# Performance work log

Hardware: AMD Instinct MI355X
Metric: run time of the kernel (lower is better)

The kernel has to match this reference:

```python
import jax, jax.numpy as jnp
import numpy as np

HIDDEN = 4096
N_HEADS = 32
N_KV_HEADS = 8
HEAD_DIM = HIDDEN // N_HEADS  # 128
ROPE_THETA = 10000.0
NEG_INF = -1e9


def rotate_half(x):
    x1, x2 = jnp.split(x, 2, axis=-1)
    return jnp.concatenate([-x2, x1], axis=-1)


def rope_cos_sin(seq_len, dim, dtype):
    inv_freq = 1.0 / (ROPE_THETA ** (jnp.arange(0, dim, 2, dtype=jnp.float32) / dim))
    t = jnp.arange(seq_len, dtype=jnp.float32)
    freqs = jnp.outer(t, inv_freq)              # (S, dim/2)
    emb = jnp.concatenate([freqs, freqs], -1)   # (S, dim)
    return jnp.cos(emb).astype(dtype), jnp.sin(emb).astype(dtype)


def setup_inputs() -> dict:
    key = jax.random.key(0)
    ks = jax.random.split(key, 5)
    B, S = 2, 2048
    hidden_states = jax.random.normal(ks[0], (B, S, HIDDEN), jnp.float32)
    # additive causal mask (B, 1, S, S)
    causal = jnp.triu(jnp.full((S, S), NEG_INF, jnp.float32), k=1)
    attention_mask = jnp.broadcast_to(causal[None, None], (B, 1, S, S))
    scale = 0.02
    wq = jax.random.normal(ks[1], (HIDDEN, HIDDEN), jnp.float32) * scale
    wk = jax.random.normal(ks[2], (N_KV_HEADS * HEAD_DIM, HIDDEN), jnp.float32) * scale
    wv = jax.random.normal(ks[3], (N_KV_HEADS * HEAD_DIM, HIDDEN), jnp.float32) * scale
    wo = jax.random.normal(ks[4], (HIDDEN, HIDDEN), jnp.float32) * scale
    return {"hidden_states": hidden_states, "attention_mask": attention_mask,
            "wq": wq, "wk": wk, "wv": wv, "wo": wo}


def reference(hidden_states, attention_mask, wq, wk, wv, wo):
    B, S, _ = hidden_states.shape
    H, Hk, D = N_HEADS, N_KV_HEADS, HEAD_DIM
    G = H // Hk  # kv groups

    q = (hidden_states @ wq.T).reshape(B, S, H, D).transpose(0, 2, 1, 3)   # (B,H,S,D)
    k = (hidden_states @ wk.T).reshape(B, S, Hk, D).transpose(0, 2, 1, 3)  # (B,Hk,S,D)
    v = (hidden_states @ wv.T).reshape(B, S, Hk, D).transpose(0, 2, 1, 3)

    cos, sin = rope_cos_sin(S, D, hidden_states.dtype)  # (S,D)
    cos = cos[None, None]  # (1,1,S,D)
    sin = sin[None, None]
    q = q * cos + rotate_half(q) * sin
    k = k * cos + rotate_half(k) * sin

    # GQA without materializing repeated K/V: view q as (B,Hk,G,S,D)
    qg = q.reshape(B, Hk, G, S, D)
    scores = jnp.einsum('bkgqd,bkld->bkgql', qg, k) / jnp.sqrt(jnp.asarray(D, q.dtype))
    scores = scores + attention_mask[:, :, None]  # (B,1,1,S,S) broadcast
    attn = jax.nn.softmax(scores.astype(jnp.float32), axis=-1).astype(q.dtype)
    out = jnp.einsum('bkgql,bkld->bkgqd', attn, v)  # (B,Hk,G,S,D)
    out = out.reshape(B, H, S, D).transpose(0, 2, 1, 3).reshape(B, S, H * D)
    return out @ wo.T
```

## Files before the change

kernel.cpp:

```cpp
#include <hip/hip_runtime.h>
#include <hip/hip_bf16.h>
#include <stdint.h>


#define HIDDEN 4096
#define NH 32
#define NKV 8
#define HD 128
#define SLEN 2048
#define BATCH 2
#define QKVLD 6144

typedef __attribute__((ext_vector_type(8))) short bf16x8;
typedef __attribute__((ext_vector_type(4))) float f32x4;

__device__ __forceinline__ unsigned short f2bf(float f) {
  __hip_bfloat16 h = __float2bfloat16(f);
  return *reinterpret_cast<unsigned short*>(&h);
}
__device__ __forceinline__ float bf2f(unsigned short h) {
  union { uint32_t u; float f; } v; v.u = ((uint32_t)h) << 16;
  return v.f;
}
__device__ __forceinline__ void gload_lds16(const void* g, void* l) {
  __builtin_amdgcn_global_load_lds(
      (const __attribute__((address_space(1))) unsigned int*)g,
      (__attribute__((address_space(3))) unsigned int*)l, 16, 0, 0);
}

__global__ __launch_bounds__(256) void cvt_f32_bf16(const float* __restrict__ in,
                                                    unsigned short* __restrict__ out) {
  size_t i = ((size_t)blockIdx.x * 256 + threadIdx.x) * 8;
  f32x4 a = *(const f32x4*)&in[i];
  f32x4 b = *(const f32x4*)&in[i + 4];
  bf16x8 o;
#pragma unroll
  for (int j = 0; j < 4; ++j) { o[j] = (short)f2bf(a[j]); o[4 + j] = (short)f2bf(b[j]); }
  *(bf16x8*)&out[i] = o;
}

__device__ __forceinline__ void store_out(unsigned short* C, size_t i, float v) { C[i] = f2bf(v); }
__device__ __forceinline__ void store_out(float* C, size_t i, float v) { C[i] = v; }

template <typename OutT>
__global__ __launch_bounds__(256, 2)
void gemm_bt(const unsigned short* __restrict__ A, const unsigned short* __restrict__ B,
             OutT* __restrict__ C, int M, int N, int K) {
  __shared__ __align__(16) unsigned short Asm[128 * 32];
  __shared__ __align__(16) unsigned short Bsm[128 * 32];
  const int tid = threadIdx.x;
  const int lane = tid & 63, wid = tid >> 6;
  const int lr = lane & 15, lg = lane >> 4;
  const int wr = wid >> 1, wc = wid & 1;

  const int nbn = N >> 7;
  const int nwg = gridDim.x;
  int wg = (int)blockIdx.x;
  wg = (wg & 7) * (nwg >> 3) + (wg >> 3);
  const int bm = wg / nbn, bn = wg % nbn;

  const unsigned short* Ab = A + (size_t)bm * 128 * K;
  const unsigned short* Bb = B + (size_t)bn * 128 * K;

  f32x4 acc[4][4] = {};

  const int c0 = tid, c1 = tid + 256;
  const int ar0 = c0 >> 2, ak0 = (c0 & 3) * 8;
  const int ar1 = c1 >> 2, ak1 = (c1 & 3) * 8;

  for (int kt = 0; kt < K; kt += 32) {
    __syncthreads();
    gload_lds16(Ab + (size_t)ar0 * K + kt + ak0, &Asm[c0 * 8]);
    gload_lds16(Ab + (size_t)ar1 * K + kt + ak1, &Asm[c1 * 8]);
    gload_lds16(Bb + (size_t)ar0 * K + kt + ak0, &Bsm[c0 * 8]);
    gload_lds16(Bb + (size_t)ar1 * K + kt + ak1, &Bsm[c1 * 8]);
    __syncthreads();

    bf16x8 af[4], bfr[4];
#pragma unroll
    for (int mi = 0; mi < 4; ++mi)
      af[mi] = *(const bf16x8*)&Asm[(wr * 64 + mi * 16 + lr) * 32 + lg * 8];
#pragma unroll
    for (int ni = 0; ni < 4; ++ni)
      bfr[ni] = *(const bf16x8*)&Bsm[(wc * 64 + ni * 16 + lr) * 32 + lg * 8];
#pragma unroll
    for (int mi = 0; mi < 4; ++mi)
#pragma unroll
      for (int ni = 0; ni < 4; ++ni)
        acc[mi][ni] = __builtin_amdgcn_mfma_f32_16x16x32_bf16(af[mi], bfr[ni], acc[mi][ni], 0, 0, 0);
  }

#pragma unroll
  for (int mi = 0; mi < 4; ++mi)
#pragma unroll
    for (int ni = 0; ni < 4; ++ni)
#pragma unroll
      for (int r = 0; r < 4; ++r) {
        size_t row = (size_t)bm * 128 + wr * 64 + mi * 16 + lg * 4 + r;
        size_t col = (size_t)bn * 128 + wc * 64 + ni * 16 + lr;
        store_out(C, row * N + col, acc[mi][ni][r]);
      }
}

__global__ __launch_bounds__(256) void rope_tables(float* __restrict__ ct, float* __restrict__ st) {
  int idx = blockIdx.x * 256 + threadIdx.x;
  int s = idx >> 6, j = idx & 63;
  float inv = exp2f(-(float)j * (13.287712379549449f / 64.f));
  float f = (float)s * inv;
  ct[idx] = cosf(f);
  st[idx] = sinf(f);
}

__global__ __launch_bounds__(256) void rope_apply(unsigned short* __restrict__ X, int ld,
                                                  const float* __restrict__ ct,
                                                  const float* __restrict__ st, int heads) {
  int idx = blockIdx.x * 256 + threadIdx.x;
  int jc = (idx & 7) * 8;
  int t2 = idx >> 3;
  int hh = t2 % heads;
  int row = t2 / heads;
  int s = row & (SLEN - 1);
  unsigned short* p = X + (size_t)row * ld + hh * HD;
  bf16x8 lo = *(bf16x8*)&p[jc];
  bf16x8 hi = *(bf16x8*)&p[64 + jc];
  bf16x8 nlo, nhi;
#pragma unroll
  for (int j = 0; j < 8; ++j) {
    float c = ct[s * 64 + jc + j];
    float sn = st[s * 64 + jc + j];
    float xl = bf2f((unsigned short)(lo[j]));
    float xh = bf2f((unsigned short)(hi[j]));
    nlo[j] = (short)f2bf(xl * c - xh * sn);
    nhi[j] = (short)f2bf(xh * c + xl * sn);
  }
  *(bf16x8*)&p[jc] = nlo;
  *(bf16x8*)&p[64 + jc] = nhi;
}

__global__ __launch_bounds__(256) void transpose_v(const unsigned short* __restrict__ Vsrc, int ld,
                                                   unsigned short* __restrict__ VT) {
  __shared__ unsigned short tile[64][66];
  const int t = threadIdx.x;
  const int bs = blockIdx.x;
  const int bd = blockIdx.y;
  const int b = bs >> 5;
  const int s0 = (bs & 31) * 64;
  const int d0 = bd * 64;
#pragma unroll
  for (int it = 0; it < 2; ++it) {
    int si = (t >> 3) + it * 32;
    int dj = (t & 7) * 8;
    bf16x8 v = *(const bf16x8*)&Vsrc[(size_t)(b * SLEN + s0 + si) * ld + d0 + dj];
#pragma unroll
    for (int j = 0; j < 8; ++j) tile[si][dj + j] = (unsigned short)(v[j]);
  }
  __syncthreads();
#pragma unroll
  for (int it = 0; it < 2; ++it) {
    int di = (t >> 3) + it * 32;
    int sj = (t & 7) * 8;
    bf16x8 o;
#pragma unroll
    for (int j = 0; j < 8; ++j) o[j] = (short)tile[sj + j][di];
    int c = d0 + di;
    int kvh = c >> 7, d = c & 127;
    *(bf16x8*)&VT[(((size_t)b * NKV + kvh) * HD + d) * SLEN + s0 + sj] = o;
  }
}

__global__ __launch_bounds__(256, 2)
void attn_fwd(const unsigned short* __restrict__ QKV, const unsigned short* __restrict__ VTm,
              unsigned short* __restrict__ Om) {
  const int blk = blockIdx.x;
  const int xcd = blk & 7, jj = blk >> 3;
  const int g = xcd + ((jj >> 5) << 3);
  const int pair = jj & 31;
  const int kvh = g & 7, b = g >> 3;
  const int tid = threadIdx.x;
  const int lane = tid & 63, w = tid >> 6;
  const int lr = lane & 15, lg = lane >> 4;
  const int h = kvh * 4 + w;

  __shared__ __align__(16) unsigned short Ksm[64 * 136];
  __shared__ __align__(16) unsigned short Vsm[128 * 72];
  __shared__ __align__(16) unsigned short Psm[4][32 * 72];
  __shared__ float Alds[4][32];

  const float SL2E = 0.1275378504229740f;

  const unsigned short* Kb0 = QKV + (size_t)(b * SLEN) * QKVLD + 4096 + kvh * HD;
  const unsigned short* VTb = VTm + ((size_t)(b * NKV + kvh) * HD) * SLEN;

#pragma unroll 1
  for (int halfq = 0; halfq < 2; ++halfq) {
    const int qt = halfq ? (63 - pair) : pair;
    const int q0 = qt * 32;
    const int ntiles = (qt >> 1) + 1;

    bf16x8 qf[2][4];
    const unsigned short* Qb = QKV + (size_t)(b * SLEN + q0) * QKVLD + h * HD;
#pragma unroll
    for (int ni = 0; ni < 2; ++ni)
#pragma unroll
      for (int kd = 0; kd < 4; ++kd)
        qf[ni][kd] = *(const bf16x8*)&Qb[(size_t)(ni * 16 + lr) * QKVLD + kd * 32 + lg * 8];

    f32x4 acc_o[2][8] = {};
    float m_run[2] = {-1e30f, -1e30f};
    float l_run[2] = {0.f, 0.f};

    bf16x8 kreg[4], vreg[4];
#pragma unroll
    for (int i = 0; i < 4; ++i) {
      int c = tid + i * 256;
      kreg[i] = *(const bf16x8*)&Kb0[(size_t)(c >> 4) * QKVLD + (c & 15) * 8];
      vreg[i] = *(const bf16x8*)&VTb[(size_t)(c >> 3) * SLEN + (c & 7) * 8];
    }

#pragma unroll 1
    for (int t = 0; t < ntiles; ++t) {
      const int kv0 = t * 64;
      __syncthreads();
#pragma unroll
      for (int i = 0; i < 4; ++i) {
        int c = tid + i * 256;
        *(bf16x8*)&Ksm[(c >> 4) * 136 + (c & 15) * 8] = kreg[i];
        *(bf16x8*)&Vsm[(c >> 3) * 72 + (c & 7) * 8] = vreg[i];
      }
      __syncthreads();

      if (t + 1 < ntiles) {
#pragma unroll
        for (int i = 0; i < 4; ++i) {
          int c = tid + i * 256;
          kreg[i] = *(const bf16x8*)&Kb0[(size_t)(kv0 + 64 + (c >> 4)) * QKVLD + (c & 15) * 8];
          vreg[i] = *(const bf16x8*)&VTb[(size_t)(c >> 3) * SLEN + kv0 + 64 + (c & 7) * 8];
        }
      }

      f32x4 accs[4][2] = {};
#pragma unroll
      for (int kd = 0; kd < 4; ++kd) {
        bf16x8 kf[4];
#pragma unroll
        for (int mi = 0; mi < 4; ++mi)
          kf[mi] = *(const bf16x8*)&Ksm[(mi * 16 + lr) * 136 + kd * 32 + lg * 8];
        __builtin_amdgcn_s_setprio(1);
#pragma unroll
        for (int mi = 0; mi < 4; ++mi)
#pragma unroll
          for (int ni = 0; ni < 2; ++ni)
            accs[mi][ni] =
                __builtin_amdgcn_mfma_f32_16x16x32_bf16(kf[mi], qf[ni][kd], accs[mi][ni], 0, 0, 0);
        __builtin_amdgcn_s_setprio(0);
      }

      const bool domask = (t == ntiles - 1);
      float alpha[2];
#pragma unroll
      for (int ni = 0; ni < 2; ++ni) {
        float cmax = -1e30f;
#pragma unroll
        for (int mi = 0; mi < 4; ++mi)
#pragma unroll
          for (int r = 0; r < 4; ++r) {
            float s = accs[mi][ni][r] * SL2E;
            if (domask) {
              int key = kv0 + mi * 16 + lg * 4 + r;
              int qq = q0 + ni * 16 + lr;
              if (key > qq) s = -1e30f;
            }
            accs[mi][ni][r] = s;
            cmax = fmaxf(cmax, s);
          }
        cmax = fmaxf(cmax, __shfl_xor(cmax, 16));
        cmax = fmaxf(cmax, __shfl_xor(cmax, 32));
        float mnew = fmaxf(m_run[ni], cmax);
        alpha[ni] = exp2f(m_run[ni] - mnew);
        float psum = 0.f;
#pragma unroll
        for (int mi = 0; mi < 4; ++mi)
#pragma unroll
          for (int r = 0; r < 4; ++r) {
            float p = exp2f(accs[mi][ni][r] - mnew);
            accs[mi][ni][r] = p;
            psum += p;
          }
        psum += __shfl_xor(psum, 16);
        psum += __shfl_xor(psum, 32);
        l_run[ni] = l_run[ni] * alpha[ni] + psum;
        m_run[ni] = mnew;
      }

      if (__any(alpha[0] < 1.f) || __any(alpha[1] < 1.f)) {
        if (lg == 0) { Alds[w][lr] = alpha[0]; Alds[w][16 + lr] = alpha[1]; }
        f32x4 al0 = *(const f32x4*)&Alds[w][lg * 4];
        f32x4 al1 = *(const f32x4*)&Alds[w][16 + lg * 4];
#pragma unroll
        for (int nd = 0; nd < 8; ++nd)
#pragma unroll
          for (int r = 0; r < 4; ++r) {
            acc_o[0][nd][r] *= al0[r];
            acc_o[1][nd][r] *= al1[r];
          }
      }

#pragma unroll
      for (int ni = 0; ni < 2; ++ni)
#pragma unroll
        for (int mi = 0; mi < 4; ++mi)
#pragma unroll
          for (int rp = 0; rp < 4; rp += 2) {
            uint32_t pk = (uint32_t)f2bf(accs[mi][ni][rp]) |
                          ((uint32_t)f2bf(accs[mi][ni][rp + 1]) << 16);
            *(uint32_t*)&Psm[w][(ni * 16 + lr) * 72 + mi * 16 + lg * 4 + rp] = pk;
          }

#pragma unroll
      for (int ks = 0; ks < 2; ++ks) {
        bf16x8 pa[2];
#pragma unroll
        for (int pm = 0; pm < 2; ++pm)
          pa[pm] = *(const bf16x8*)&Psm[w][(pm * 16 + lr) * 72 + ks * 32 + lg * 8];
        __builtin_amdgcn_s_setprio(1);
#pragma unroll
        for (int nd = 0; nd < 8; ++nd) {
          bf16x8 vb = *(const bf16x8*)&Vsm[(nd * 16 + lr) * 72 + ks * 32 + lg * 8];
#pragma unroll
          for (int pm = 0; pm < 2; ++pm)
            acc_o[pm][nd] =
                __builtin_amdgcn_mfma_f32_16x16x32_bf16(pa[pm], vb, acc_o[pm][nd], 0, 0, 0);
        }
        __builtin_amdgcn_s_setprio(0);
      }
    }

    if (lg == 0) {
      Alds[w][lr] = 1.f / l_run[0];
      Alds[w][16 + lr] = 1.f / l_run[1];
    }
    f32x4 li0 = *(const f32x4*)&Alds[w][lg * 4];
    f32x4 li1 = *(const f32x4*)&Alds[w][16 + lg * 4];
    unsigned short* Ob = Om + ((size_t)(b * SLEN + q0) * NH + h) * HD;
#pragma unroll
    for (int pm = 0; pm < 2; ++pm)
#pragma unroll
      for (int nd = 0; nd < 8; ++nd)
#pragma unroll
        for (int r = 0; r < 4; ++r) {
          int qq = pm * 16 + lg * 4 + r;
          float v = acc_o[pm][nd][r] * (pm ? li1[r] : li0[r]);
          Ob[(size_t)qq * (NH * HD) + nd * 16 + lr] = f2bf(v);
        }
  }
}

extern "C" void kernel_launch(void* const* d_in, const int* in_sizes, int n_in,
                              void* d_out, int out_size, void* d_ws, size_t ws_size,
                              hipStream_t stream) {
  const float* hidden = (const float*)d_in[0];
  const float* wq = (const float*)d_in[2];
  const float* wk = (const float*)d_in[3];
  const float* wv = (const float*)d_in[4];
  const float* wo = (const float*)d_in[5];

  char* ws = (char*)d_ws;
  const size_t MB = 1ull << 20;
  unsigned short* Xbf  = (unsigned short*)(ws);
  unsigned short* Wqkv = (unsigned short*)(ws + 32 * MB);
  unsigned short* QKV  = (unsigned short*)(ws + 80 * MB);
  unsigned short* Ob   = (unsigned short*)(ws + 128 * MB);
  unsigned short* VTb  = (unsigned short*)(ws + 160 * MB);
  float* ct = (float*)(ws + 168 * MB);
  float* st = (float*)(ws + 168 * MB + 524288);

  cvt_f32_bf16<<<8192, 256, 0, stream>>>(hidden, Xbf);
  cvt_f32_bf16<<<8192, 256, 0, stream>>>(wq, Wqkv);
  cvt_f32_bf16<<<2048, 256, 0, stream>>>(wk, Wqkv + (size_t)4096 * 4096);
  cvt_f32_bf16<<<2048, 256, 0, stream>>>(wv, Wqkv + (size_t)5120 * 4096);

  gemm_bt<unsigned short><<<1536, 256, 0, stream>>>(Xbf, Wqkv, QKV, 4096, 6144, 4096);

  rope_tables<<<512, 256, 0, stream>>>(ct, st);
  rope_apply<<<4096, 256, 0, stream>>>(QKV, QKVLD, ct, st, NH);
  rope_apply<<<1024, 256, 0, stream>>>(QKV + 4096, QKVLD, ct, st, NKV);

  transpose_v<<<dim3(64, 16), 256, 0, stream>>>(QKV + 5120, QKVLD, VTb);

  attn_fwd<<<512, 256, 0, stream>>>(QKV, VTb, Ob);

  cvt_f32_bf16<<<8192, 256, 0, stream>>>(wo, Wqkv);
  gemm_bt<float><<<1024, 256, 0, stream>>>(Ob, Wqkv, (float*)d_out, 4096, 4096, 4096);
}
```

Measured before the change: 650.6 us.

## Use 256x256 GEMM tiles with four-stage LDS prefetch pipeline

Replaces the 128x128 single-buffered GEMM with a 512-thread 256x256 tile kernel that prefetches three K-slices ahead into a four-buffer LDS ring. Loads are tracked with explicit vmcnt waits and a single barrier per iteration, and MFMA sections run at raised wave priority. This is meant to hide global-load latency and raise data reuse per tile. In exchange it uses 128 KB of LDS per block, which limits occupancy, and the 384-block QKV grid leaves a partial wave.

```diff
diff --git a/kernel.cpp b/kernel.cpp
--- a/kernel.cpp
+++ b/kernel.cpp
@@ -43,61 +43,91 @@
 __device__ __forceinline__ void store_out(float* C, size_t i, float v) { C[i] = v; }
 
 template <typename OutT>
-__global__ __launch_bounds__(256, 2)
-void gemm_bt(const unsigned short* __restrict__ A, const unsigned short* __restrict__ B,
-             OutT* __restrict__ C, int M, int N, int K) {
-  __shared__ __align__(16) unsigned short Asm[128 * 32];
-  __shared__ __align__(16) unsigned short Bsm[128 * 32];
+__global__ __launch_bounds__(512, 2)
+void gemm_bt256(const unsigned short* __restrict__ A, const unsigned short* __restrict__ B,
+                OutT* __restrict__ C, int M, int N, int K) {
+  __shared__ __align__(16) unsigned short lds[4 * 2048 * 8];
+
   const int tid = threadIdx.x;
-  const int lane = tid & 63, wid = tid >> 6;
+  const int lane = tid & 63, w = tid >> 6;
   const int lr = lane & 15, lg = lane >> 4;
-  const int wr = wid >> 1, wc = wid & 1;
-
-  const int nbn = N >> 7;
+  const int wr = w >> 2, wc = w & 3;
+
+  const int nbn = N >> 8;
   const int nwg = gridDim.x;
   int wg = (int)blockIdx.x;
   wg = (wg & 7) * (nwg >> 3) + (wg >> 3);
   const int bm = wg / nbn, bn = wg % nbn;
 
-  const unsigned short* Ab = A + (size_t)bm * 128 * K;
-  const unsigned short* Bb = B + (size_t)bn * 128 * K;
-
-  f32x4 acc[4][4] = {};
-
-  const int c0 = tid, c1 = tid + 256;
-  const int ar0 = c0 >> 2, ak0 = (c0 & 3) * 8;
-  const int ar1 = c1 >> 2, ak1 = (c1 & 3) * 8;
-
-  for (int kt = 0; kt < K; kt += 32) {
-    __syncthreads();
-    gload_lds16(Ab + (size_t)ar0 * K + kt + ak0, &Asm[c0 * 8]);
-    gload_lds16(Ab + (size_t)ar1 * K + kt + ak1, &Asm[c1 * 8]);
-    gload_lds16(Bb + (size_t)ar0 * K + kt + ak0, &Bsm[c0 * 8]);
-    gload_lds16(Bb + (size_t)ar1 * K + kt + ak1, &Bsm[c1 * 8]);
-    __syncthreads();
-
-    bf16x8 af[4], bfr[4];
-#pragma unroll
-    for (int mi = 0; mi < 4; ++mi)
-      af[mi] = *(const bf16x8*)&Asm[(wr * 64 + mi * 16 + lr) * 32 + lg * 8];
+  const unsigned short* Ab = A + (size_t)bm * 256 * K;
+  const unsigned short* Bb = B + (size_t)bn * 256 * K;
+
+  f32x4 acc[8][4] = {};
+
+  auto stage = [&](int t2) {
+    const int kt = t2 * 32;
+    unsigned short* lb = lds + (size_t)(t2 & 3) * 2048 * 8;
+#pragma unroll
+    for (int j = 0; j < 2; ++j) {
+      int idx = tid + j * 512;
+      gload_lds16(Ab + (size_t)(idx >> 2) * K + kt + (idx & 3) * 8,
+                  lb + (size_t)(w * 64 + j * 512) * 8);
+    }
+#pragma unroll
+    for (int j = 0; j < 2; ++j) {
+      int idx = tid + j * 512;
+      gload_lds16(Bb + (size_t)(idx >> 2) * K + kt + (idx & 3) * 8,
+                  lb + (size_t)(1024 + w * 64 + j * 512) * 8);
+    }
+  };
+
+  const int NT = K >> 5;
+
+  stage(0);
+  stage(1);
+  stage(2);
+  asm volatile("s_waitcnt vmcnt(8)" ::: "memory");
+  __builtin_amdgcn_s_barrier();
+  asm volatile("" ::: "memory");
+
+#pragma unroll 1
+  for (int t = 0; t < NT; ++t) {
+    if (t + 3 < NT) stage(t + 3);
+
+    const unsigned short* bufp = lds + (size_t)(t & 3) * 2048 * 8;
+    bf16x8 af[8], bfv[4];
+#pragma unroll
+    for (int mi = 0; mi < 8; ++mi)
+      af[mi] = *(const bf16x8*)&bufp[(size_t)(wr * 512 + mi * 64 + lr * 4 + lg) * 8];
 #pragma unroll
     for (int ni = 0; ni < 4; ++ni)
-      bfr[ni] = *(const bf16x8*)&Bsm[(wc * 64 + ni * 16 + lr) * 32 + lg * 8];
-#pragma unroll
-    for (int mi = 0; mi < 4; ++mi)
+      bfv[ni] = *(const bf16x8*)&bufp[(size_t)(1024 + wc * 256 + ni * 64 + lr * 4 + lg) * 8];
+
+    __builtin_amdgcn_s_setprio(1);
+#pragma unroll
+    for (int mi = 0; mi < 8; ++mi)
 #pragma unroll
       for (int ni = 0; ni < 4; ++ni)
-        acc[mi][ni] = __builtin_amdgcn_mfma_f32_16x16x32_bf16(af[mi], bfr[ni], acc[mi][ni], 0, 0, 0);
+        acc[mi][ni] = __builtin_amdgcn_mfma_f32_16x16x32_bf16(af[mi], bfv[ni], acc[mi][ni], 0, 0, 0);
+    __builtin_amdgcn_s_setprio(0);
+
+    if (t + 1 < NT) {
+      if (t + 3 < NT)      asm volatile("s_waitcnt vmcnt(8)" ::: "memory");
+      else if (t + 2 < NT) asm volatile("s_waitcnt vmcnt(4)" ::: "memory");
+      else                 asm volatile("s_waitcnt vmcnt(0)" ::: "memory");
+      __builtin_amdgcn_s_barrier();
+      asm volatile("" ::: "memory");
+    }
   }
 
 #pragma unroll
-  for (int mi = 0; mi < 4; ++mi)
+  for (int mi = 0; mi < 8; ++mi)
 #pragma unroll
     for (int ni = 0; ni < 4; ++ni)
 #pragma unroll
       for (int r = 0; r < 4; ++r) {
-        size_t row = (size_t)bm * 128 + wr * 64 + mi * 16 + lg * 4 + r;
-        size_t col = (size_t)bn * 128 + wc * 64 + ni * 16 + lr;
+        size_t row = (size_t)bm * 256 + wr * 128 + mi * 16 + lg * 4 + r;
+        size_t col = (size_t)bn * 256 + wc * 64 + ni * 16 + lr;
         store_out(C, row * N + col, acc[mi][ni][r]);
       }
 }
@@ -379,7 +409,7 @@
   cvt_f32_bf16<<<2048, 256, 0, stream>>>(wk, Wqkv + (size_t)4096 * 4096);
   cvt_f32_bf16<<<2048, 256, 0, stream>>>(wv, Wqkv + (size_t)5120 * 4096);
 
-  gemm_bt<unsigned short><<<1536, 256, 0, stream>>>(Xbf, Wqkv, QKV, 4096, 6144, 4096);
+  gemm_bt256<unsigned short><<<384, 512, 0, stream>>>(Xbf, Wqkv, QKV, 4096, 6144, 4096);
 
   rope_tables<<<512, 256, 0, stream>>>(ct, st);
   rope_apply<<<4096, 256, 0, stream>>>(QKV, QKVLD, ct, st, NH);
@@ -390,5 +420,5 @@
   attn_fwd<<<512, 256, 0, stream>>>(QKV, VTb, Ob);
 
   cvt_f32_bf16<<<8192, 256, 0, stream>>>(wo, Wqkv);
-  gemm_bt<float><<<1024, 256, 0, stream>>>(Ob, Wqkv, (float*)d_out, 4096, 4096, 4096);
-}
+  gemm_bt256<float><<<256, 512, 0, stream>>>(Ob, Wqkv, (float*)d_out, 4096, 4096, 4096);
+}
```

After: 601.1 us. 1.08x faster.
